# Performance work log

Hardware: AMD Instinct MI355X
Metric: run time of the kernel (lower is better)

Reference implementation:

```python
import jax, jax.numpy as jnp
import numpy as np
from functools import partial

GRAD_THR = 0.01
COUNT_THR = 3
MIN_PROB = 0.1
MAX_PROB = 0.9
FREE_PROB = 1e-10
HEIGHT_Q = 0.7


def prob2logodds(p):
    return jnp.log(p) - jnp.log1p(-p)


def shift_diff(x, d):
    # right neighbor minus left neighbor at dilation d (replicate padding on width)
    xp = jnp.pad(x, [(0, 0)] * (x.ndim - 1) + [(d, d)], mode='edge')
    return xp[..., 2 * d:] - xp[..., :-2 * d]


def assign_score(depth):
    rml_dx = jax.nn.relu(shift_diff(depth, 1))    # relu(right - left)
    lmr_dx = jax.nn.relu(-shift_diff(depth, 1))   # relu(left - right)
    rml_ddx = jax.nn.relu(-shift_diff(rml_dx, 2))  # relu(-(right-left))
    lmr_ddx = jax.nn.relu(shift_diff(lmr_dx, 2))   # relu(-(left-right))
    W = depth.shape[-1]
    grad_pos = jnp.concatenate([rml_ddx[..., :W // 2], lmr_ddx[..., W // 2:]], axis=-1)
    grad_neg = jnp.concatenate([lmr_ddx[..., :W // 2], rml_ddx[..., W // 2:]], axis=-1)
    return grad_pos, grad_neg


def _occupancy_one(xyz, score, g_mask, size, grad_thr, count_thr):
    # xyz: [3, N]; score, g_mask: [N]
    x, y, z = xyz[0], xyz[1], xyz[2]
    range_mask = (x >= 0) & (x <= size - 1) & (z >= 0) & (z <= size - 1)
    height_mask = y < jnp.quantile(y, HEIGHT_Q)
    valid = height_mask & range_mask
    obj = valid & (~g_mask) & (score > 0)
    ground = valid & g_mask
    xi = jnp.clip(x.astype(jnp.int32), 0, size - 1)
    zi = jnp.clip(z.astype(jnp.int32), 0, size - 1)
    idx = xi + size * zi  # [N] flat grid index
    G = size * size
    occ = jnp.zeros(G, jnp.float32).at[idx].add(
        jnp.where(obj & (score > grad_thr), 1.0, 0.0))
    norm = jnp.zeros(G, jnp.float32).at[idx].add(obj.astype(jnp.float32))
    gcnt = jnp.zeros(G, jnp.float32).at[idx].add(ground.astype(jnp.float32))
    free = (gcnt > 0) & (norm == 0)
    unknown = (~free) & (norm < count_thr)
    prob = occ / jnp.maximum(norm, 1.0)
    prob = jnp.where(unknown | free, 0.5, prob)
    return prob, free, unknown


def compute_occupancy_probability(scaled_ptcloud, ground_flat, disc_flat, size, grad_thr, count_thr):
    f = partial(_occupancy_one, size=size, grad_thr=grad_thr, count_thr=count_thr)
    return jax.vmap(f)(scaled_ptcloud, disc_flat, ground_flat)


def max_pool3x3(x):
    return jax.lax.reduce_window(
        x, -jnp.inf, jax.lax.max,
        (1, 1, 3, 3), (1, 1, 1, 1),
        [(0, 0), (0, 0), (1, 1), (1, 1)])


def setup_inputs() -> dict:
    key = jax.random.key(0)
    k1, k2, k3 = jax.random.split(key, 3)
    B, H, W, S = 32, 384, 1280, 256
    N = H * W
    depth = jax.random.uniform(k1, (B, 1, H, W), jnp.float32, 0.1, 80.0)
    ptc = jax.random.uniform(k2, (B, 3, N), jnp.float32, -5.0, float(S) + 5.0)
    gmask = jax.random.randint(k3, (B, 1, H, W), 0, 2).astype(bool)
    return {"depth": depth, "scaled_ptcloud": ptc, "ground_mask": gmask, "ogm_size": S}


def reference(depth, scaled_ptcloud, ground_mask, ogm_size):
    B = depth.shape[0]
    S = ogm_size
    prior_free_odds = prob2logodds(FREE_PROB)
    p_min_odds = prob2logodds(MIN_PROB)
    p_max_odds = prob2logodds(MAX_PROB)
    n_max_odds = prob2logodds(MAX_PROB)

    grad_pos, grad_neg = assign_score(depth)
    gp_flat = grad_pos.reshape(B, -1)
    gn_flat = grad_neg.reshape(B, -1)
    gm_flat = ground_mask.reshape(B, -1)

    pos_prob, free, unknown = compute_occupancy_probability(
        scaled_ptcloud, gm_flat, gp_flat, S, GRAD_THR, COUNT_THR)
    pos_odds = prob2logodds(pos_prob)
    pos_odds = jnp.where(free, prior_free_odds, pos_odds)
    pos_odds = jnp.where(unknown, 0.0, pos_odds)
    pos_odds = jnp.clip(pos_odds, p_min_odds, p_max_odds)

    neg_prob, _, _ = compute_occupancy_probability(
        scaled_ptcloud, gm_flat, gn_flat, S, GRAD_THR, COUNT_THR)
    neg_odds = prob2logodds(neg_prob)
    neg_odds = jnp.where(free | unknown, 0.0, neg_odds)
    neg_odds = jnp.clip(neg_odds, 0.0, n_max_odds)
    neg_odds = max_pool3x3(neg_odds.reshape(B, 1, S, S))

    return pos_odds.reshape(B, 1, S, S) - neg_odds
```

## Files before the change

### kernel.cpp

```cpp
#include <hip/hip_runtime.h>
#include <stdint.h>

#define H_    384
#define W_    1280
#define NPTS  (H_ * W_)
#define S_    256
#define G_    (S_ * S_)
#define NBX   32
#define NBINS 4096
#define QCAP  2048
#define LO_   (-16.0f)
#define INVW_ (4096.0f / 544.0f)
#define PMAX  2.1972246f

typedef unsigned int u32;
typedef unsigned long long u64;
typedef unsigned char u8;
typedef float f32x4 __attribute__((ext_vector_type(4)));
typedef u32   u32x4 __attribute__((ext_vector_type(4)));

__device__ __forceinline__ u32 fkey(float f) {
    u32 u = __float_as_uint(f);
    return (u & 0x80000000u) ? ~u : (u | 0x80000000u);
}
__device__ __forceinline__ float keyfloat(u32 k) {
    u32 u = (k & 0x80000000u) ? (k ^ 0x80000000u) : ~k;
    return __uint_as_float(u);
}
__device__ __forceinline__ int lbin(float y) {
    int b = (int)floorf((y - LO_) * INVW_);
    return b < 0 ? 0 : (b > NBINS - 1 ? NBINS - 1 : b);
}

__global__ void k_histlin(const float* __restrict__ ptc, const u8* __restrict__ gmb,
                          u32* __restrict__ hgsum, u32* __restrict__ mode) {
    __shared__ u32 h[NBINS];
    const int t = threadIdx.x, b = blockIdx.y;
    if (blockIdx.x == 0 && b == 0 && t < 64) {
        u32 v = ((const u32*)gmb)[t];
        bool bad = !(v == 0u || v == 1u || v == 0x3F800000u);
        u64 m = __ballot(bad);
        if (t == 0) *mode = (m == 0ULL) ? 1u : 0u;
    }
    for (int j = t; j < NBINS; j += 256) h[j] = 0u;
    __syncthreads();
    const f32x4* y4 = (const f32x4*)(ptc + (size_t)b * 3 * NPTS + NPTS);
    for (int i = blockIdx.x * 256 + t; i < NPTS / 4; i += NBX * 256) {
        f32x4 v = y4[i];
        atomicAdd(&h[lbin(v.x)], 1u);
        atomicAdd(&h[lbin(v.y)], 1u);
        atomicAdd(&h[lbin(v.z)], 1u);
        atomicAdd(&h[lbin(v.w)], 1u);
    }
    __syncthreads();
    u32* dst = hgsum + (size_t)b * NBINS;
    for (int j = t; j < NBINS; j += 256)
        if (h[j]) atomicAdd(&dst[j], h[j]);
}

__global__ void k_find(const u32* __restrict__ hgsum, u32* __restrict__ fbuf, int ka) {
    __shared__ u32 h[NBINS];
    __shared__ u32 part[256];
    __shared__ u32 sres[4];
    const int t = threadIdx.x, b = blockIdx.x;
    const u32* src = hgsum + (size_t)b * NBINS;
    for (int j = t; j < NBINS; j += 256) h[j] = src[j];
    __syncthreads();
    u32 loc = 0;
#pragma unroll
    for (int q = 0; q < NBINS / 256; q++) loc += h[t * (NBINS / 256) + q];
    part[t] = loc;
    __syncthreads();
    for (int ofs = 1; ofs < 256; ofs <<= 1) {
        u32 v = (t >= ofs) ? part[t - ofs] : 0u;
        __syncthreads();
        part[t] += v;
        __syncthreads();
    }
    u32 before = part[t] - loc;
    const u32 ra = (u32)ka, rb = (u32)ka + 1u;
#pragma unroll
    for (int q = 0; q < NBINS / 256; q++) {
        const int j = t * (NBINS / 256) + q;
        const u32 v = h[j];
        if (before <= ra && ra < before + v) { sres[0] = (u32)j; sres[1] = ra - before; }
        if (before <= rb && rb < before + v) { sres[2] = (u32)j; sres[3] = rb - before; }
        before += v;
    }
    __syncthreads();
    if (t < 4) fbuf[b * 4 + t] = sres[t];
}

__global__ void k_collect(const float* __restrict__ ptc, const u32* __restrict__ fbuf,
                          u32* __restrict__ cnt, u32* __restrict__ cbuf) {
    __shared__ u32 sA, sB;
    const int t = threadIdx.x, b = blockIdx.y;
    if (t == 0) { sA = fbuf[b * 4 + 0]; sB = fbuf[b * 4 + 2]; }
    __syncthreads();
    const int binA = (int)sA, binB = (int)sB;
    const bool twob = (binB != binA);
    const f32x4* y4 = (const f32x4*)(ptc + (size_t)b * 3 * NPTS + NPTS);
    u32* bufA = cbuf + (size_t)b * 2 * QCAP;
    u32* bufB = bufA + QCAP;
    for (int i = blockIdx.x * 256 + t; i < NPTS / 4; i += NBX * 256) {
        f32x4 v = y4[i];
        float f[4] = {v.x, v.y, v.z, v.w};
#pragma unroll
        for (int q = 0; q < 4; q++) {
            const int bn = lbin(f[q]);
            if (bn == binA) {
                u32 p = atomicAdd(&cnt[b * 2], 1u);
                if (p < QCAP) bufA[p] = fkey(f[q]);
            } else if (twob && bn == binB) {
                u32 p = atomicAdd(&cnt[b * 2 + 1], 1u);
                if (p < QCAP) bufB[p] = fkey(f[q]);
            }
        }
    }
}

__global__ void k_select(const u32* __restrict__ fbuf, const u32* __restrict__ cnt,
                         const u32* __restrict__ cbuf, float* __restrict__ tbuf,
                         float wlo, float whi) {
    __shared__ u32 sA[QCAP];
    __shared__ u32 sB[QCAP];
    __shared__ u32 skey[2];
    const int t = threadIdx.x, b = blockIdx.x;
    const u32 binA = fbuf[b * 4 + 0], remA = fbuf[b * 4 + 1];
    const u32 binB = fbuf[b * 4 + 2], remB = fbuf[b * 4 + 3];
    const bool twob = (binB != binA);
    u32 cA = cnt[b * 2];     if (cA > QCAP) cA = QCAP;
    u32 cB = cnt[b * 2 + 1]; if (cB > QCAP) cB = QCAP;
    const u32* bufA = cbuf + (size_t)b * 2 * QCAP;
    const u32* bufB = bufA + QCAP;
    for (u32 i = t; i < cA; i += 256) sA[i] = bufA[i];
    if (twob) for (u32 i = t; i < cB; i += 256) sB[i] = bufB[i];
    __syncthreads();
    for (u32 i = t; i < cA; i += 256) {
        const u32 k = sA[i];
        u32 less = 0, eq = 0;
        for (u32 j = 0; j < cA; j++) { u32 kj = sA[j]; less += (kj < k); eq += (kj == k); }
        if (less <= remA && remA < less + eq) skey[0] = k;
    }
    const u32* src = twob ? sB : sA;
    const u32 mB = twob ? cB : cA;
    for (u32 i = t; i < mB; i += 256) {
        const u32 k = src[i];
        u32 less = 0, eq = 0;
        for (u32 j = 0; j < mB; j++) { u32 kj = src[j]; less += (kj < k); eq += (kj == k); }
        if (less <= remB && remB < less + eq) skey[1] = k;
    }
    __syncthreads();
    if (t == 0) {
        float ylo = keyfloat(skey[0]);
        float yhi = keyfloat(skey[1]);
        tbuf[b] = __fadd_rn(__fmul_rn(ylo, wlo), __fmul_rn(yhi, whi));
    }
    (void)binA;
}

__global__ void k_scatter(const float* __restrict__ depth, const float* __restrict__ ptc,
                          const u8* __restrict__ gmb, const float* __restrict__ tbuf,
                          const u32* __restrict__ mode,
                          u32* __restrict__ pk, u8* __restrict__ gflag) {
    __shared__ float st;
    __shared__ u32 smode;
    if (threadIdx.x == 0) { st = tbuf[blockIdx.y]; smode = *mode; }
    __syncthreads();
    const int b = blockIdx.y;
    const int i4 = blockIdx.x * 256 + threadIdx.x;
    const int i0 = i4 * 4;
    const size_t pb = (size_t)b * 3 * NPTS;

    const f32x4 yv = __builtin_nontemporal_load((const f32x4*)(ptc + pb + NPTS) + i4);
    const float fy[4] = {yv.x, yv.y, yv.z, yv.w};
    bool pass[4]; bool any = false;
#pragma unroll
    for (int q = 0; q < 4; q++) { pass[q] = fy[q] < st; any = any || pass[q]; }
    if (!any) return;

    const f32x4 xv = __builtin_nontemporal_load((const f32x4*)(ptc + pb) + i4);
    const f32x4 zv = __builtin_nontemporal_load((const f32x4*)(ptc + pb + 2 * NPTS) + i4);
    const float fx[4] = {xv.x, xv.y, xv.z, xv.w};
    const float fz[4] = {zv.x, zv.y, zv.z, zv.w};
    u32 gw[4];
    if (smode) {
        u32x4 gg = __builtin_nontemporal_load((const u32x4*)((const u32*)gmb + (size_t)b * NPTS) + i4);
        gw[0] = gg.x; gw[1] = gg.y; gw[2] = gg.z; gw[3] = gg.w;
    } else {
        u32 gg = __builtin_nontemporal_load((const u32*)(gmb + (size_t)b * NPTS) + i4);
        gw[0] = gg & 0xFFu; gw[1] = (gg >> 8) & 0xFFu; gw[2] = (gg >> 16) & 0xFFu; gw[3] = (gg >> 24) & 0xFFu;
    }

    const int colbase = i0 % W_;
    const float* drow = depth + (size_t)b * NPTS + (i0 - colbase);
    u32* pkb = pk + (size_t)b * G_;
    u8* gfb = gflag + (size_t)b * G_;

#pragma unroll
    for (int q = 0; q < 4; q++) {
        if (!pass[q]) continue;
        const float x = fx[q], z = fz[q];
        if (!(x >= 0.0f && x <= 255.0f && z >= 0.0f && z <= 255.0f)) continue;
        const int cell = (int)x + S_ * (int)z;
        if (gw[q]) { gfb[cell] = 1; continue; }

        const int col = colbase + q;
        int j1 = col - 2; if (j1 < 0) j1 = 0;
        int j2 = col + 2; if (j2 > W_ - 1) j2 = W_ - 1;
        int am = j1 - 1;  if (am < 0) am = 0;
        int ap = j1 + 1;  if (ap > W_ - 1) ap = W_ - 1;
        int bm = j2 - 1;  if (bm < 0) bm = 0;
        int bp = j2 + 1;  if (bp > W_ - 1) bp = W_ - 1;
        float a = drow[ap] - drow[am];
        float c = drow[bp] - drow[bm];
        float rml1 = fmaxf(a, 0.0f),  lmr1 = fmaxf(-a, 0.0f);
        float rml2 = fmaxf(c, 0.0f),  lmr2 = fmaxf(-c, 0.0f);
        float rddx = fmaxf(rml1 - rml2, 0.0f);
        float lddx = fmaxf(lmr2 - lmr1, 0.0f);
        float sp, sn;
        if (col < W_ / 2) { sp = rddx; sn = lddx; } else { sp = lddx; sn = rddx; }
        u32 p = (sp > 0.0f) ? (1u | ((u32)(sp > 0.01f) << 8)) : 0u;
        u32 n = (sn > 0.0f) ? ((1u << 16) | ((u32)(sn > 0.01f) << 24)) : 0u;
        const u32 inc = p | n;
        if (inc) atomicAdd(&pkb[cell], inc);
    }
}

#define TX 64
#define TZ 16

__device__ __forceinline__ float neg_val(u32 w) {
    const u32 pn = w & 0xFFu;
    if (pn < 3u) return 0.0f;
    const u32 nn = (w >> 16) & 0xFFu;
    if (nn < 3u) return 0.0f;
    const u32 no = (w >> 24) & 0xFFu;
    float p = (float)no / (float)nn;
    float v = logf(p) - log1pf(-p);
    return fminf(fmaxf(v, 0.0f), PMAX);
}

__global__ void k_finalpool(const u32* __restrict__ pk, const u8* __restrict__ gflag,
                            float* __restrict__ out) {
    __shared__ float ng[(TZ + 2) * (TX + 2)];
    const int t = threadIdx.x, b = blockIdx.y;
    const int x0 = (blockIdx.x & 3) * TX;
    const int z0 = (blockIdx.x >> 2) * TZ;
    const u32* pkb = pk + (size_t)b * G_;
    const u8* gfb = gflag + (size_t)b * G_;
    for (int idx = t; idx < (TZ + 2) * (TX + 2); idx += 256) {
        const int gx = x0 + idx % (TX + 2) - 1;
        const int gz = z0 + idx / (TX + 2) - 1;
        float v = -INFINITY;
        if (gx >= 0 && gx < S_ && gz >= 0 && gz < S_) v = neg_val(pkb[gx + S_ * gz]);
        ng[idx] = v;
    }
    __syncthreads();
    const int lx = t & 63;
    const int lz0 = (t >> 6) * 4;
#pragma unroll
    for (int k = 0; k < 4; k++) {
        const int lz = lz0 + k;
        const int cell = (x0 + lx) + S_ * (z0 + lz);
        const u32 w = pkb[cell];
        const u32 pn = w & 0xFFu;
        float po;
        if (pn < 3u) {
            po = (pn == 0u && gfb[cell]) ? -PMAX : 0.0f;
        } else {
            const u32 oc = (w >> 8) & 0xFFu;
            float p = (float)oc / (float)pn;
            float v = logf(p) - log1pf(-p);
            po = fminf(fmaxf(v, -PMAX), PMAX);
        }
        float mx = -INFINITY;
#pragma unroll
        for (int dz = 0; dz < 3; dz++)
#pragma unroll
            for (int dx = 0; dx < 3; dx++)
                mx = fmaxf(mx, ng[(lz + dz) * (TX + 2) + (lx + dx)]);
        out[(size_t)b * G_ + cell] = po - mx;
    }
}

extern "C" void kernel_launch(void* const* d_in, const int* in_sizes, int n_in,
                              void* d_out, int out_size, void* d_ws, size_t ws_size,
                              hipStream_t stream) {
    const float* depth = (const float*)d_in[0];
    const float* ptc   = (const float*)d_in[1];
    const u8* gm       = (const u8*)d_in[2];
    const int B = in_sizes[0] / NPTS;

    char* ws = (char*)d_ws;
    size_t off = 0;
    auto alloc = [&](size_t bytes) -> void* {
        void* p = ws + off; off += (bytes + 255) & ~(size_t)255; return p;
    };
    u32* pk    = (u32*)alloc((size_t)B * G_ * 4);
    u8*  gflag = (u8*)alloc((size_t)B * G_);
    u32* hgsum = (u32*)alloc((size_t)B * NBINS * 4);
    u32* cnt   = (u32*)alloc((size_t)B * 2 * 4);
    const size_t zero_bytes = off;
    u32* cbuf  = (u32*)alloc((size_t)B * 2 * QCAP * 4);
    float* tbuf= (float*)alloc((size_t)B * 4);
    u32* fbuf  = (u32*)alloc((size_t)B * 4 * 4);
    u32* mode  = (u32*)alloc(4);
    (void)ws_size; (void)n_in; (void)out_size;

    (void)hipMemsetAsync(d_ws, 0, zero_bytes, stream);

    const float idxf = 0.7f * (float)(NPTS - 1);
    const int   ka   = (int)floorf(idxf);
    const float whi  = idxf - (float)ka;
    const float wlo  = 1.0f - whi;

    k_histlin <<<dim3(NBX, B), dim3(256), 0, stream>>>(ptc, gm, hgsum, mode);
    k_find    <<<dim3(B), dim3(256), 0, stream>>>(hgsum, fbuf, ka);
    k_collect <<<dim3(NBX, B), dim3(256), 0, stream>>>(ptc, fbuf, cnt, cbuf);
    k_select  <<<dim3(B), dim3(256), 0, stream>>>(fbuf, cnt, cbuf, tbuf, wlo, whi);
    k_scatter <<<dim3(NPTS / 1024, B), dim3(256), 0, stream>>>(
        depth, ptc, gm, tbuf, mode, pk, gflag);
    k_finalpool<<<dim3(64, B), dim3(256), 0, stream>>>(pk, gflag, (float*)d_out);
}
```

Measured before the change: 507.9 us.

## Fuse all phases into one cooperative persistent kernel with grid syncs

Replaces the memset plus six separate launches with a single cooperative kernel that runs zeroing, histogram, quantile find and collect, select, scatter and final pooling as phases separated by grid-wide syncs. Each block covers a fixed batch and slice, and the scatter phase becomes a grid-stride loop. The quantile bin search is recomputed per block instead of stored, and select buffers reuse shared memory. The aim is to remove launch and inter-kernel gaps, at the cost of grid barrier overhead, a fixed block count limited by occupancy, and a fallback multi-kernel path if the cooperative launch fails.

```diff
diff --git a/kernel.cpp b/kernel.cpp
--- a/kernel.cpp
+++ b/kernel.cpp
@@ -1,17 +1,22 @@
 #include <hip/hip_runtime.h>
+#include <hip/hip_cooperative_groups.h>
 #include <stdint.h>
+
+namespace cg = cooperative_groups;
 
 #define H_    384
 #define W_    1280
 #define NPTS  (H_ * W_)
 #define S_    256
 #define G_    (S_ * S_)
-#define NBX   32
+#define NBB   64
 #define NBINS 4096
-#define QCAP  2048
+#define QCAP  1024
 #define LO_   (-16.0f)
 #define INVW_ (4096.0f / 544.0f)
 #define PMAX  2.1972246f
+#define TX 64
+#define TZ 16
 
 typedef unsigned int u32;
 typedef unsigned long long u64;
@@ -19,6 +24,15 @@
 typedef float f32x4 __attribute__((ext_vector_type(4)));
 typedef u32   u32x4 __attribute__((ext_vector_type(4)));
 
+struct Shm {
+    u32 h[NBINS];
+    u32 part[256];
+    u32 sres[4];
+    u32 skey[2];
+    float sth;
+    u32 smode;
+};
+
 __device__ __forceinline__ u32 fkey(float f) {
     u32 u = __float_as_uint(f);
     return (u & 0x80000000u) ? ~u : (u | 0x80000000u);
@@ -31,78 +45,77 @@
     int b = (int)floorf((y - LO_) * INVW_);
     return b < 0 ? 0 : (b > NBINS - 1 ? NBINS - 1 : b);
 }
-
-__global__ void k_histlin(const float* __restrict__ ptc, const u8* __restrict__ gmb,
-                          u32* __restrict__ hgsum, u32* __restrict__ mode) {
-    __shared__ u32 h[NBINS];
-    const int t = threadIdx.x, b = blockIdx.y;
-    if (blockIdx.x == 0 && b == 0 && t < 64) {
-        u32 v = ((const u32*)gmb)[t];
-        bool bad = !(v == 0u || v == 1u || v == 0x3F800000u);
-        u64 m = __ballot(bad);
-        if (t == 0) *mode = (m == 0ULL) ? 1u : 0u;
-    }
-    for (int j = t; j < NBINS; j += 256) h[j] = 0u;
+__device__ __forceinline__ void decode(int id, int& b, int& j) {
+    const int r = id & 7;
+    const int g8 = id >> 3;
+    j = g8 % NBB;
+    b = (g8 / NBB) * 8 + r;
+}
+
+__device__ void phase_zero(int b, int j, int t, u32* pk, u8* gflag, u32* hgsum, u32* cnt) {
+    const u32x4 z4 = {0u, 0u, 0u, 0u};
+    u32x4* pk4 = (u32x4*)(pk + (size_t)b * G_) + (size_t)j * (G_ / 4 / NBB);
+    for (int k = t; k < G_ / 4 / NBB; k += 256) pk4[k] = z4;
+    u32x4* gf4 = (u32x4*)(gflag + (size_t)b * G_) + (size_t)j * (G_ / 16 / NBB);
+    for (int k = t; k < G_ / 16 / NBB; k += 256) gf4[k] = z4;
+    u32* hs = hgsum + (size_t)b * NBINS + j * (NBINS / NBB);
+    for (int k = t; k < NBINS / NBB; k += 256) hs[k] = 0u;
+    if (j == 0 && t < 2) cnt[b * 2 + t] = 0u;
+}
+
+__device__ void phase_hist(int b, int j, int t, const float* ptc, u32* hgsum, Shm& s) {
+    for (int k = t; k < NBINS; k += 256) s.h[k] = 0u;
     __syncthreads();
     const f32x4* y4 = (const f32x4*)(ptc + (size_t)b * 3 * NPTS + NPTS);
-    for (int i = blockIdx.x * 256 + t; i < NPTS / 4; i += NBX * 256) {
+    for (int i = j * 256 + t; i < NPTS / 4; i += NBB * 256) {
         f32x4 v = y4[i];
-        atomicAdd(&h[lbin(v.x)], 1u);
-        atomicAdd(&h[lbin(v.y)], 1u);
-        atomicAdd(&h[lbin(v.z)], 1u);
-        atomicAdd(&h[lbin(v.w)], 1u);
+        atomicAdd(&s.h[lbin(v.x)], 1u);
+        atomicAdd(&s.h[lbin(v.y)], 1u);
+        atomicAdd(&s.h[lbin(v.z)], 1u);
+        atomicAdd(&s.h[lbin(v.w)], 1u);
     }
     __syncthreads();
     u32* dst = hgsum + (size_t)b * NBINS;
-    for (int j = t; j < NBINS; j += 256)
-        if (h[j]) atomicAdd(&dst[j], h[j]);
-}
-
-__global__ void k_find(const u32* __restrict__ hgsum, u32* __restrict__ fbuf, int ka) {
-    __shared__ u32 h[NBINS];
-    __shared__ u32 part[256];
-    __shared__ u32 sres[4];
-    const int t = threadIdx.x, b = blockIdx.x;
+    for (int k = t; k < NBINS; k += 256)
+        if (s.h[k]) atomicAdd(&dst[k], s.h[k]);
+}
+
+__device__ void phase_find(int b, int t, const u32* hgsum, int ka, Shm& s) {
     const u32* src = hgsum + (size_t)b * NBINS;
-    for (int j = t; j < NBINS; j += 256) h[j] = src[j];
+    for (int k = t; k < NBINS; k += 256) s.h[k] = src[k];
     __syncthreads();
     u32 loc = 0;
 #pragma unroll
-    for (int q = 0; q < NBINS / 256; q++) loc += h[t * (NBINS / 256) + q];
-    part[t] = loc;
+    for (int q = 0; q < NBINS / 256; q++) loc += s.h[t * (NBINS / 256) + q];
+    s.part[t] = loc;
     __syncthreads();
     for (int ofs = 1; ofs < 256; ofs <<= 1) {
-        u32 v = (t >= ofs) ? part[t - ofs] : 0u;
+        u32 v = (t >= ofs) ? s.part[t - ofs] : 0u;
         __syncthreads();
-        part[t] += v;
+        s.part[t] += v;
         __syncthreads();
     }
-    u32 before = part[t] - loc;
+    u32 before = s.part[t] - loc;
     const u32 ra = (u32)ka, rb = (u32)ka + 1u;
 #pragma unroll
     for (int q = 0; q < NBINS / 256; q++) {
-        const int j = t * (NBINS / 256) + q;
-        const u32 v = h[j];
-        if (before <= ra && ra < before + v) { sres[0] = (u32)j; sres[1] = ra - before; }
-        if (before <= rb && rb < before + v) { sres[2] = (u32)j; sres[3] = rb - before; }
+        const int jj = t * (NBINS / 256) + q;
+        const u32 v = s.h[jj];
+        if (before <= ra && ra < before + v) { s.sres[0] = (u32)jj; s.sres[1] = ra - before; }
+        if (before <= rb && rb < before + v) { s.sres[2] = (u32)jj; s.sres[3] = rb - before; }
         before += v;
     }
     __syncthreads();
-    if (t < 4) fbuf[b * 4 + t] = sres[t];
-}
-
-__global__ void k_collect(const float* __restrict__ ptc, const u32* __restrict__ fbuf,
-                          u32* __restrict__ cnt, u32* __restrict__ cbuf) {
-    __shared__ u32 sA, sB;
-    const int t = threadIdx.x, b = blockIdx.y;
-    if (t == 0) { sA = fbuf[b * 4 + 0]; sB = fbuf[b * 4 + 2]; }
-    __syncthreads();
-    const int binA = (int)sA, binB = (int)sB;
+}
+
+__device__ void phase_collect(int b, int j, int t, const float* ptc,
+                              u32* cnt, u32* cbuf, Shm& s) {
+    const int binA = (int)s.sres[0], binB = (int)s.sres[2];
     const bool twob = (binB != binA);
     const f32x4* y4 = (const f32x4*)(ptc + (size_t)b * 3 * NPTS + NPTS);
     u32* bufA = cbuf + (size_t)b * 2 * QCAP;
     u32* bufB = bufA + QCAP;
-    for (int i = blockIdx.x * 256 + t; i < NPTS / 4; i += NBX * 256) {
+    for (int i = j * 256 + t; i < NPTS / 4; i += NBB * 256) {
         f32x4 v = y4[i];
         float f[4] = {v.x, v.y, v.z, v.w};
 #pragma unroll
@@ -119,116 +132,114 @@
     }
 }
 
-__global__ void k_select(const u32* __restrict__ fbuf, const u32* __restrict__ cnt,
-                         const u32* __restrict__ cbuf, float* __restrict__ tbuf,
-                         float wlo, float whi) {
-    __shared__ u32 sA[QCAP];
-    __shared__ u32 sB[QCAP];
-    __shared__ u32 skey[2];
-    const int t = threadIdx.x, b = blockIdx.x;
-    const u32 binA = fbuf[b * 4 + 0], remA = fbuf[b * 4 + 1];
-    const u32 binB = fbuf[b * 4 + 2], remB = fbuf[b * 4 + 3];
-    const bool twob = (binB != binA);
+__device__ void phase_select(int b, int t, const u32* cnt, const u32* cbuf,
+                             float* tbuf, float wlo, float whi, Shm& s) {
+    const u32 remA = s.sres[1], remB = s.sres[3];
+    const bool twob = (s.sres[0] != s.sres[2]);
     u32 cA = cnt[b * 2];     if (cA > QCAP) cA = QCAP;
     u32 cB = cnt[b * 2 + 1]; if (cB > QCAP) cB = QCAP;
     const u32* bufA = cbuf + (size_t)b * 2 * QCAP;
     const u32* bufB = bufA + QCAP;
+    u32* sA = s.h;
+    u32* sB = s.h + QCAP;
+    __syncthreads();
     for (u32 i = t; i < cA; i += 256) sA[i] = bufA[i];
     if (twob) for (u32 i = t; i < cB; i += 256) sB[i] = bufB[i];
     __syncthreads();
     for (u32 i = t; i < cA; i += 256) {
         const u32 k = sA[i];
         u32 less = 0, eq = 0;
-        for (u32 j = 0; j < cA; j++) { u32 kj = sA[j]; less += (kj < k); eq += (kj == k); }
-        if (less <= remA && remA < less + eq) skey[0] = k;
-    }
-    const u32* src = twob ? sB : sA;
+        for (u32 jj = 0; jj < cA; jj++) { u32 kj = sA[jj]; less += (kj < k); eq += (kj == k); }
+        if (less <= remA && remA < less + eq) s.skey[0] = k;
+    }
+    const u32* srcb = twob ? sB : sA;
     const u32 mB = twob ? cB : cA;
     for (u32 i = t; i < mB; i += 256) {
-        const u32 k = src[i];
+        const u32 k = srcb[i];
         u32 less = 0, eq = 0;
-        for (u32 j = 0; j < mB; j++) { u32 kj = src[j]; less += (kj < k); eq += (kj == k); }
-        if (less <= remB && remB < less + eq) skey[1] = k;
+        for (u32 jj = 0; jj < mB; jj++) { u32 kj = srcb[jj]; less += (kj < k); eq += (kj == k); }
+        if (less <= remB && remB < less + eq) s.skey[1] = k;
     }
     __syncthreads();
     if (t == 0) {
-        float ylo = keyfloat(skey[0]);
-        float yhi = keyfloat(skey[1]);
+        float ylo = keyfloat(s.skey[0]);
+        float yhi = keyfloat(s.skey[1]);
         tbuf[b] = __fadd_rn(__fmul_rn(ylo, wlo), __fmul_rn(yhi, whi));
     }
-    (void)binA;
-}
-
-__global__ void k_scatter(const float* __restrict__ depth, const float* __restrict__ ptc,
-                          const u8* __restrict__ gmb, const float* __restrict__ tbuf,
-                          const u32* __restrict__ mode,
-                          u32* __restrict__ pk, u8* __restrict__ gflag) {
-    __shared__ float st;
-    __shared__ u32 smode;
-    if (threadIdx.x == 0) { st = tbuf[blockIdx.y]; smode = *mode; }
-    __syncthreads();
-    const int b = blockIdx.y;
-    const int i4 = blockIdx.x * 256 + threadIdx.x;
-    const int i0 = i4 * 4;
+}
+
+__device__ void phase_scatter(int b, int j, int t, const float* depth, const float* ptc,
+                              const u8* gmb, const float* tbuf,
+                              u32* pk, u8* gflag, Shm& s) {
+    if (t < 64) {
+        u32 v = ((const u32*)gmb)[t];
+        bool bad = !(v == 0u || v == 1u || v == 0x3F800000u);
+        u64 m = __ballot(bad);
+        if (t == 0) s.smode = (m == 0ULL) ? 1u : 0u;
+    }
+    if (t == 0) s.sth = tbuf[b];
+    __syncthreads();
+    const float st = s.sth;
+    const u32 smode = s.smode;
     const size_t pb = (size_t)b * 3 * NPTS;
-
-    const f32x4 yv = __builtin_nontemporal_load((const f32x4*)(ptc + pb + NPTS) + i4);
-    const float fy[4] = {yv.x, yv.y, yv.z, yv.w};
-    bool pass[4]; bool any = false;
-#pragma unroll
-    for (int q = 0; q < 4; q++) { pass[q] = fy[q] < st; any = any || pass[q]; }
-    if (!any) return;
-
-    const f32x4 xv = __builtin_nontemporal_load((const f32x4*)(ptc + pb) + i4);
-    const f32x4 zv = __builtin_nontemporal_load((const f32x4*)(ptc + pb + 2 * NPTS) + i4);
-    const float fx[4] = {xv.x, xv.y, xv.z, xv.w};
-    const float fz[4] = {zv.x, zv.y, zv.z, zv.w};
-    u32 gw[4];
-    if (smode) {
-        u32x4 gg = __builtin_nontemporal_load((const u32x4*)((const u32*)gmb + (size_t)b * NPTS) + i4);
-        gw[0] = gg.x; gw[1] = gg.y; gw[2] = gg.z; gw[3] = gg.w;
-    } else {
-        u32 gg = __builtin_nontemporal_load((const u32*)(gmb + (size_t)b * NPTS) + i4);
-        gw[0] = gg & 0xFFu; gw[1] = (gg >> 8) & 0xFFu; gw[2] = (gg >> 16) & 0xFFu; gw[3] = (gg >> 24) & 0xFFu;
-    }
-
-    const int colbase = i0 % W_;
-    const float* drow = depth + (size_t)b * NPTS + (i0 - colbase);
     u32* pkb = pk + (size_t)b * G_;
     u8* gfb = gflag + (size_t)b * G_;
 
-#pragma unroll
-    for (int q = 0; q < 4; q++) {
-        if (!pass[q]) continue;
-        const float x = fx[q], z = fz[q];
-        if (!(x >= 0.0f && x <= 255.0f && z >= 0.0f && z <= 255.0f)) continue;
-        const int cell = (int)x + S_ * (int)z;
-        if (gw[q]) { gfb[cell] = 1; continue; }
-
-        const int col = colbase + q;
-        int j1 = col - 2; if (j1 < 0) j1 = 0;
-        int j2 = col + 2; if (j2 > W_ - 1) j2 = W_ - 1;
-        int am = j1 - 1;  if (am < 0) am = 0;
-        int ap = j1 + 1;  if (ap > W_ - 1) ap = W_ - 1;
-        int bm = j2 - 1;  if (bm < 0) bm = 0;
-        int bp = j2 + 1;  if (bp > W_ - 1) bp = W_ - 1;
-        float a = drow[ap] - drow[am];
-        float c = drow[bp] - drow[bm];
-        float rml1 = fmaxf(a, 0.0f),  lmr1 = fmaxf(-a, 0.0f);
-        float rml2 = fmaxf(c, 0.0f),  lmr2 = fmaxf(-c, 0.0f);
-        float rddx = fmaxf(rml1 - rml2, 0.0f);
-        float lddx = fmaxf(lmr2 - lmr1, 0.0f);
-        float sp, sn;
-        if (col < W_ / 2) { sp = rddx; sn = lddx; } else { sp = lddx; sn = rddx; }
-        u32 p = (sp > 0.0f) ? (1u | ((u32)(sp > 0.01f) << 8)) : 0u;
-        u32 n = (sn > 0.0f) ? ((1u << 16) | ((u32)(sn > 0.01f) << 24)) : 0u;
-        const u32 inc = p | n;
-        if (inc) atomicAdd(&pkb[cell], inc);
-    }
-}
-
-#define TX 64
-#define TZ 16
+    for (int i4 = j * 256 + t; i4 < NPTS / 4; i4 += NBB * 256) {
+        const int i0 = i4 * 4;
+        const f32x4 yv = __builtin_nontemporal_load((const f32x4*)(ptc + pb + NPTS) + i4);
+        const float fy[4] = {yv.x, yv.y, yv.z, yv.w};
+        bool pass[4]; bool any = false;
+#pragma unroll
+        for (int q = 0; q < 4; q++) { pass[q] = fy[q] < st; any = any || pass[q]; }
+        if (!any) continue;
+
+        const f32x4 xv = __builtin_nontemporal_load((const f32x4*)(ptc + pb) + i4);
+        const f32x4 zv = __builtin_nontemporal_load((const f32x4*)(ptc + pb + 2 * NPTS) + i4);
+        const float fx[4] = {xv.x, xv.y, xv.z, xv.w};
+        const float fz[4] = {zv.x, zv.y, zv.z, zv.w};
+        u32 gw[4];
+        if (smode) {
+            u32x4 gg = __builtin_nontemporal_load((const u32x4*)((const u32*)gmb + (size_t)b * NPTS) + i4);
+            gw[0] = gg.x; gw[1] = gg.y; gw[2] = gg.z; gw[3] = gg.w;
+        } else {
+            u32 gg = __builtin_nontemporal_load((const u32*)(gmb + (size_t)b * NPTS) + i4);
+            gw[0] = gg & 0xFFu; gw[1] = (gg >> 8) & 0xFFu; gw[2] = (gg >> 16) & 0xFFu; gw[3] = (gg >> 24) & 0xFFu;
+        }
+
+        const int colbase = i0 % W_;
+        const float* drow = depth + (size_t)b * NPTS + (i0 - colbase);
+
+#pragma unroll
+        for (int q = 0; q < 4; q++) {
+            if (!pass[q]) continue;
+            const float x = fx[q], z = fz[q];
+            if (!(x >= 0.0f && x <= 255.0f && z >= 0.0f && z <= 255.0f)) continue;
+            const int cell = (int)x + S_ * (int)z;
+            if (gw[q]) { gfb[cell] = 1; continue; }
+
+            const int col = colbase + q;
+            int j1 = col - 2; if (j1 < 0) j1 = 0;
+            int j2 = col + 2; if (j2 > W_ - 1) j2 = W_ - 1;
+            int am = j1 - 1;  if (am < 0) am = 0;
+            int ap = j1 + 1;  if (ap > W_ - 1) ap = W_ - 1;
+            int bm = j2 - 1;  if (bm < 0) bm = 0;
+            int bp = j2 + 1;  if (bp > W_ - 1) bp = W_ - 1;
+            float a = drow[ap] - drow[am];
+            float c = drow[bp] - drow[bm];
+            float rml1 = fmaxf(a, 0.0f),  lmr1 = fmaxf(-a, 0.0f);
+            float rml2 = fmaxf(c, 0.0f),  lmr2 = fmaxf(-c, 0.0f);
+            float rddx = fmaxf(rml1 - rml2, 0.0f);
+            float lddx = fmaxf(lmr2 - lmr1, 0.0f);
+            float sp, sn;
+            if (col < W_ / 2) { sp = rddx; sn = lddx; } else { sp = lddx; sn = rddx; }
+            u32 p = (sp > 0.0f) ? (1u | ((u32)(sp > 0.01f) << 8)) : 0u;
+            u32 n = (sn > 0.0f) ? ((1u << 16) | ((u32)(sn > 0.01f) << 24)) : 0u;
+            const u32 inc = p | n;
+            if (inc) atomicAdd(&pkb[cell], inc);
+        }
+    }
+}
 
 __device__ __forceinline__ float neg_val(u32 w) {
     const u32 pn = w & 0xFFu;
@@ -241,14 +252,14 @@
     return fminf(fmaxf(v, 0.0f), PMAX);
 }
 
-__global__ void k_finalpool(const u32* __restrict__ pk, const u8* __restrict__ gflag,
-                            float* __restrict__ out) {
-    __shared__ float ng[(TZ + 2) * (TX + 2)];
-    const int t = threadIdx.x, b = blockIdx.y;
-    const int x0 = (blockIdx.x & 3) * TX;
-    const int z0 = (blockIdx.x >> 2) * TZ;
+__device__ void phase_final(int b, int j, int t, const u32* pk, const u8* gflag,
+                            float* out, Shm& s) {
+    float* ng = (float*)s.h;
+    const int x0 = (j & 3) * TX;
+    const int z0 = (j >> 2) * TZ;
     const u32* pkb = pk + (size_t)b * G_;
     const u8* gfb = gflag + (size_t)b * G_;
+    __syncthreads();
     for (int idx = t; idx < (TZ + 2) * (TX + 2); idx += 256) {
         const int gx = x0 + idx % (TX + 2) - 1;
         const int gz = z0 + idx / (TX + 2) - 1;
@@ -284,6 +295,62 @@
     }
 }
 
+__global__ __launch_bounds__(256, 8) void k_mega(
+        const float* __restrict__ depth, const float* __restrict__ ptc,
+        const u8* __restrict__ gmb, u32* __restrict__ pk, u8* __restrict__ gflag,
+        u32* __restrict__ hgsum, u32* __restrict__ cnt, u32* __restrict__ cbuf,
+        float* __restrict__ tbuf, float* __restrict__ out,
+        int ka, float wlo, float whi) {
+    __shared__ Shm s;
+    cg::grid_group gg = cg::this_grid();
+    int b, j; decode((int)blockIdx.x, b, j);
+    const int t = (int)threadIdx.x;
+
+    phase_zero(b, j, t, pk, gflag, hgsum, cnt);
+    gg.sync();
+    phase_hist(b, j, t, ptc, hgsum, s);
+    gg.sync();
+    phase_find(b, t, hgsum, ka, s);
+    phase_collect(b, j, t, ptc, cnt, cbuf, s);
+    gg.sync();
+    if (j == 0) phase_select(b, t, cnt, cbuf, tbuf, wlo, whi, s);
+    gg.sync();
+    phase_scatter(b, j, t, depth, ptc, gmb, tbuf, pk, gflag, s);
+    gg.sync();
+    phase_final(b, j, t, pk, gflag, out, s);
+}
+
+__global__ void k_p0(u32* pk, u8* gflag, u32* hgsum, u32* cnt) {
+    int b, j; decode((int)blockIdx.x, b, j);
+    phase_zero(b, j, (int)threadIdx.x, pk, gflag, hgsum, cnt);
+}
+__global__ void k_p1(const float* __restrict__ ptc, u32* hgsum) {
+    __shared__ Shm s; int b, j; decode((int)blockIdx.x, b, j);
+    phase_hist(b, j, (int)threadIdx.x, ptc, hgsum, s);
+}
+__global__ void k_p2(const float* __restrict__ ptc, const u32* hgsum,
+                     u32* cnt, u32* cbuf, int ka) {
+    __shared__ Shm s; int b, j; decode((int)blockIdx.x, b, j);
+    phase_find(b, (int)threadIdx.x, hgsum, ka, s);
+    phase_collect(b, j, (int)threadIdx.x, ptc, cnt, cbuf, s);
+}
+__global__ void k_p3(const u32* hgsum, const u32* cnt, const u32* cbuf,
+                     float* tbuf, int ka, float wlo, float whi) {
+    __shared__ Shm s; const int b = (int)blockIdx.x;
+    phase_find(b, (int)threadIdx.x, hgsum, ka, s);
+    phase_select(b, (int)threadIdx.x, cnt, cbuf, tbuf, wlo, whi, s);
+}
+__global__ void k_p4(const float* __restrict__ depth, const float* __restrict__ ptc,
+                     const u8* __restrict__ gmb, const float* __restrict__ tbuf,
+                     u32* pk, u8* gflag) {
+    __shared__ Shm s; int b, j; decode((int)blockIdx.x, b, j);
+    phase_scatter(b, j, (int)threadIdx.x, depth, ptc, gmb, tbuf, pk, gflag, s);
+}
+__global__ void k_p5(const u32* pk, const u8* gflag, float* out) {
+    __shared__ Shm s; int b, j; decode((int)blockIdx.x, b, j);
+    phase_final(b, j, (int)threadIdx.x, pk, gflag, out, s);
+}
+
 extern "C" void kernel_launch(void* const* d_in, const int* in_sizes, int n_in,
                               void* d_out, int out_size, void* d_ws, size_t ws_size,
                               hipStream_t stream) {
@@ -291,6 +358,7 @@
     const float* ptc   = (const float*)d_in[1];
     const u8* gm       = (const u8*)d_in[2];
     const int B = in_sizes[0] / NPTS;
+    float* outp = (float*)d_out;
 
     char* ws = (char*)d_ws;
     size_t off = 0;
@@ -301,25 +369,27 @@
     u8*  gflag = (u8*)alloc((size_t)B * G_);
     u32* hgsum = (u32*)alloc((size_t)B * NBINS * 4);
     u32* cnt   = (u32*)alloc((size_t)B * 2 * 4);
-    const size_t zero_bytes = off;
     u32* cbuf  = (u32*)alloc((size_t)B * 2 * QCAP * 4);
     float* tbuf= (float*)alloc((size_t)B * 4);
-    u32* fbuf  = (u32*)alloc((size_t)B * 4 * 4);
-    u32* mode  = (u32*)alloc(4);
     (void)ws_size; (void)n_in; (void)out_size;
 
-    (void)hipMemsetAsync(d_ws, 0, zero_bytes, stream);
-
     const float idxf = 0.7f * (float)(NPTS - 1);
-    const int   ka   = (int)floorf(idxf);
-    const float whi  = idxf - (float)ka;
-    const float wlo  = 1.0f - whi;
-
-    k_histlin <<<dim3(NBX, B), dim3(256), 0, stream>>>(ptc, gm, hgsum, mode);
-    k_find    <<<dim3(B), dim3(256), 0, stream>>>(hgsum, fbuf, ka);
-    k_collect <<<dim3(NBX, B), dim3(256), 0, stream>>>(ptc, fbuf, cnt, cbuf);
-    k_select  <<<dim3(B), dim3(256), 0, stream>>>(fbuf, cnt, cbuf, tbuf, wlo, whi);
-    k_scatter <<<dim3(NPTS / 1024, B), dim3(256), 0, stream>>>(
-        depth, ptc, gm, tbuf, mode, pk, gflag);
-    k_finalpool<<<dim3(64, B), dim3(256), 0, stream>>>(pk, gflag, (float*)d_out);
-}
+    int   ka   = (int)floorf(idxf);
+    float whi  = idxf - (float)ka;
+    float wlo  = 1.0f - whi;
+
+    void* kargs[] = { (void*)&depth, (void*)&ptc, (void*)&gm, (void*)&pk, (void*)&gflag,
+                      (void*)&hgsum, (void*)&cnt, (void*)&cbuf, (void*)&tbuf, (void*)&outp,
+                      (void*)&ka, (void*)&wlo, (void*)&whi };
+    hipError_t ce = hipLaunchCooperativeKernel((const void*)k_mega, dim3(NBB * B),
+                                               dim3(256), kargs, 0, stream);
+    if (ce != hipSuccess) {
+        (void)hipGetLastError();
+        k_p0<<<dim3(NBB * B), dim3(256), 0, stream>>>(pk, gflag, hgsum, cnt);
+        k_p1<<<dim3(NBB * B), dim3(256), 0, stream>>>(ptc, hgsum);
+        k_p2<<<dim3(NBB * B), dim3(256), 0, stream>>>(ptc, hgsum, cnt, cbuf, ka);
+        k_p3<<<dim3(B),       dim3(256), 0, stream>>>(hgsum, cnt, cbuf, tbuf, ka, wlo, whi);
+        k_p4<<<dim3(NBB * B), dim3(256), 0, stream>>>(depth, ptc, gm, tbuf, pk, gflag);
+        k_p5<<<dim3(NBB * B), dim3(256), 0, stream>>>(pk, gflag, outp);
+    }
+}
```

After: 1.536 ms. 202% more time.

## Fuse grid zeroing into histogram kernel and remap blocks across batches

Applied to the files above, without the earlier changes.

The large memset of the occupancy grid and ground flags is replaced by having each histogram block zero its own slice, so the memset now covers only the small histogram and counter buffers. All kernels switch to a 1D grid with a decode that interleaves 8 batches per group of blocks, which changes block-to-XCD placement and may improve cache locality. The candidate buffer capacity is halved, which shrinks shared memory in the select kernel but raises the chance of dropping candidates if a bin overflows.

```diff
diff --git a/kernel.cpp b/kernel.cpp
--- a/kernel.cpp
+++ b/kernel.cpp
@@ -6,12 +6,17 @@
 #define NPTS  (H_ * W_)
 #define S_    256
 #define G_    (S_ * S_)
-#define NBX   32
+#define NBH   32
+#define NBC   32
+#define NBS   480
+#define NBF   64
 #define NBINS 4096
-#define QCAP  2048
+#define QCAP  1024
 #define LO_   (-16.0f)
 #define INVW_ (4096.0f / 544.0f)
 #define PMAX  2.1972246f
+#define TX 64
+#define TZ 16
 
 typedef unsigned int u32;
 typedef unsigned long long u64;
@@ -31,21 +36,37 @@
     int b = (int)floorf((y - LO_) * INVW_);
     return b < 0 ? 0 : (b > NBINS - 1 ? NBINS - 1 : b);
 }
-
-__global__ void k_histlin(const float* __restrict__ ptc, const u8* __restrict__ gmb,
-                          u32* __restrict__ hgsum, u32* __restrict__ mode) {
+template<int NBB>
+__device__ __forceinline__ void decode(int id, int& b, int& j) {
+    const int r = id & 7;
+    const int g8 = id >> 3;
+    j = g8 % NBB;
+    b = (g8 / NBB) * 8 + r;
+}
+
+__global__ void k_hist(const float* __restrict__ ptc, const u8* __restrict__ gmb,
+                       u32* __restrict__ hgsum, u32* __restrict__ mode,
+                       u32* __restrict__ pk, u8* __restrict__ gflag) {
     __shared__ u32 h[NBINS];
-    const int t = threadIdx.x, b = blockIdx.y;
-    if (blockIdx.x == 0 && b == 0 && t < 64) {
+    int b, j; decode<NBH>((int)blockIdx.x, b, j);
+    const int t = threadIdx.x;
+    if (b == 0 && j == 0 && t < 64) {
         u32 v = ((const u32*)gmb)[t];
         bool bad = !(v == 0u || v == 1u || v == 0x3F800000u);
         u64 m = __ballot(bad);
         if (t == 0) *mode = (m == 0ULL) ? 1u : 0u;
     }
-    for (int j = t; j < NBINS; j += 256) h[j] = 0u;
+    {
+        const u32x4 z4 = {0u, 0u, 0u, 0u};
+        u32x4* pk4 = (u32x4*)(pk + (size_t)b * G_) + (size_t)j * (G_ / 4 / NBH);
+        for (int k = t; k < G_ / 4 / NBH; k += 256) pk4[k] = z4;
+        u32x4* gf4 = (u32x4*)(gflag + (size_t)b * G_) + (size_t)j * (G_ / 16 / NBH);
+        if (t < G_ / 16 / NBH) gf4[t] = z4;
+    }
+    for (int k = t; k < NBINS; k += 256) h[k] = 0u;
     __syncthreads();
     const f32x4* y4 = (const f32x4*)(ptc + (size_t)b * 3 * NPTS + NPTS);
-    for (int i = blockIdx.x * 256 + t; i < NPTS / 4; i += NBX * 256) {
+    for (int i = j * 256 + t; i < NPTS / 4; i += NBH * 256) {
         f32x4 v = y4[i];
         atomicAdd(&h[lbin(v.x)], 1u);
         atomicAdd(&h[lbin(v.y)], 1u);
@@ -54,8 +75,8 @@
     }
     __syncthreads();
     u32* dst = hgsum + (size_t)b * NBINS;
-    for (int j = t; j < NBINS; j += 256)
-        if (h[j]) atomicAdd(&dst[j], h[j]);
+    for (int k = t; k < NBINS; k += 256)
+        if (h[k]) atomicAdd(&dst[k], h[k]);
 }
 
 __global__ void k_find(const u32* __restrict__ hgsum, u32* __restrict__ fbuf, int ka) {
@@ -64,7 +85,7 @@
     __shared__ u32 sres[4];
     const int t = threadIdx.x, b = blockIdx.x;
     const u32* src = hgsum + (size_t)b * NBINS;
-    for (int j = t; j < NBINS; j += 256) h[j] = src[j];
+    for (int k = t; k < NBINS; k += 256) h[k] = src[k];
     __syncthreads();
     u32 loc = 0;
 #pragma unroll
@@ -81,10 +102,10 @@
     const u32 ra = (u32)ka, rb = (u32)ka + 1u;
 #pragma unroll
     for (int q = 0; q < NBINS / 256; q++) {
-        const int j = t * (NBINS / 256) + q;
-        const u32 v = h[j];
-        if (before <= ra && ra < before + v) { sres[0] = (u32)j; sres[1] = ra - before; }
-        if (before <= rb && rb < before + v) { sres[2] = (u32)j; sres[3] = rb - before; }
+        const int jj = t * (NBINS / 256) + q;
+        const u32 v = h[jj];
+        if (before <= ra && ra < before + v) { sres[0] = (u32)jj; sres[1] = ra - before; }
+        if (before <= rb && rb < before + v) { sres[2] = (u32)jj; sres[3] = rb - before; }
         before += v;
     }
     __syncthreads();
@@ -93,16 +114,15 @@
 
 __global__ void k_collect(const float* __restrict__ ptc, const u32* __restrict__ fbuf,
                           u32* __restrict__ cnt, u32* __restrict__ cbuf) {
-    __shared__ u32 sA, sB;
-    const int t = threadIdx.x, b = blockIdx.y;
-    if (t == 0) { sA = fbuf[b * 4 + 0]; sB = fbuf[b * 4 + 2]; }
-    __syncthreads();
-    const int binA = (int)sA, binB = (int)sB;
+    int b, j; decode<NBC>((int)blockIdx.x, b, j);
+    const int t = threadIdx.x;
+    const int binA = (int)fbuf[b * 4 + 0];
+    const int binB = (int)fbuf[b * 4 + 2];
     const bool twob = (binB != binA);
     const f32x4* y4 = (const f32x4*)(ptc + (size_t)b * 3 * NPTS + NPTS);
     u32* bufA = cbuf + (size_t)b * 2 * QCAP;
     u32* bufB = bufA + QCAP;
-    for (int i = blockIdx.x * 256 + t; i < NPTS / 4; i += NBX * 256) {
+    for (int i = j * 256 + t; i < NPTS / 4; i += NBC * 256) {
         f32x4 v = y4[i];
         float f[4] = {v.x, v.y, v.z, v.w};
 #pragma unroll
@@ -126,9 +146,8 @@
     __shared__ u32 sB[QCAP];
     __shared__ u32 skey[2];
     const int t = threadIdx.x, b = blockIdx.x;
-    const u32 binA = fbuf[b * 4 + 0], remA = fbuf[b * 4 + 1];
-    const u32 binB = fbuf[b * 4 + 2], remB = fbuf[b * 4 + 3];
-    const bool twob = (binB != binA);
+    const u32 remA = fbuf[b * 4 + 1], remB = fbuf[b * 4 + 3];
+    const bool twob = (fbuf[b * 4 + 0] != fbuf[b * 4 + 2]);
     u32 cA = cnt[b * 2];     if (cA > QCAP) cA = QCAP;
     u32 cB = cnt[b * 2 + 1]; if (cB > QCAP) cB = QCAP;
     const u32* bufA = cbuf + (size_t)b * 2 * QCAP;
@@ -139,15 +158,15 @@
     for (u32 i = t; i < cA; i += 256) {
         const u32 k = sA[i];
         u32 less = 0, eq = 0;
-        for (u32 j = 0; j < cA; j++) { u32 kj = sA[j]; less += (kj < k); eq += (kj == k); }
+        for (u32 jj = 0; jj < cA; jj++) { u32 kj = sA[jj]; less += (kj < k); eq += (kj == k); }
         if (less <= remA && remA < less + eq) skey[0] = k;
     }
-    const u32* src = twob ? sB : sA;
+    const u32* srcb = twob ? sB : sA;
     const u32 mB = twob ? cB : cA;
     for (u32 i = t; i < mB; i += 256) {
-        const u32 k = src[i];
+        const u32 k = srcb[i];
         u32 less = 0, eq = 0;
-        for (u32 j = 0; j < mB; j++) { u32 kj = src[j]; less += (kj < k); eq += (kj == k); }
+        for (u32 jj = 0; jj < mB; jj++) { u32 kj = srcb[jj]; less += (kj < k); eq += (kj == k); }
         if (less <= remB && remB < less + eq) skey[1] = k;
     }
     __syncthreads();
@@ -156,19 +175,17 @@
         float yhi = keyfloat(skey[1]);
         tbuf[b] = __fadd_rn(__fmul_rn(ylo, wlo), __fmul_rn(yhi, whi));
     }
-    (void)binA;
 }
 
 __global__ void k_scatter(const float* __restrict__ depth, const float* __restrict__ ptc,
                           const u8* __restrict__ gmb, const float* __restrict__ tbuf,
                           const u32* __restrict__ mode,
                           u32* __restrict__ pk, u8* __restrict__ gflag) {
-    __shared__ float st;
-    __shared__ u32 smode;
-    if (threadIdx.x == 0) { st = tbuf[blockIdx.y]; smode = *mode; }
-    __syncthreads();
-    const int b = blockIdx.y;
-    const int i4 = blockIdx.x * 256 + threadIdx.x;
+    int b, j; decode<NBS>((int)blockIdx.x, b, j);
+    const int t = threadIdx.x;
+    const float st = tbuf[b];
+    const u32 smode = *mode;
+    const int i4 = j * 256 + t;
     const int i0 = i4 * 4;
     const size_t pb = (size_t)b * 3 * NPTS;
 
@@ -227,9 +244,6 @@
     }
 }
 
-#define TX 64
-#define TZ 16
-
 __device__ __forceinline__ float neg_val(u32 w) {
     const u32 pn = w & 0xFFu;
     if (pn < 3u) return 0.0f;
@@ -244,9 +258,10 @@
 __global__ void k_finalpool(const u32* __restrict__ pk, const u8* __restrict__ gflag,
                             float* __restrict__ out) {
     __shared__ float ng[(TZ + 2) * (TX + 2)];
-    const int t = threadIdx.x, b = blockIdx.y;
-    const int x0 = (blockIdx.x & 3) * TX;
-    const int z0 = (blockIdx.x >> 2) * TZ;
+    int b, j; decode<NBF>((int)blockIdx.x, b, j);
+    const int t = threadIdx.x;
+    const int x0 = (j & 3) * TX;
+    const int z0 = (j >> 2) * TZ;
     const u32* pkb = pk + (size_t)b * G_;
     const u8* gfb = gflag + (size_t)b * G_;
     for (int idx = t; idx < (TZ + 2) * (TX + 2); idx += 256) {
@@ -297,11 +312,11 @@
     auto alloc = [&](size_t bytes) -> void* {
         void* p = ws + off; off += (bytes + 255) & ~(size_t)255; return p;
     };
-    u32* pk    = (u32*)alloc((size_t)B * G_ * 4);
-    u8*  gflag = (u8*)alloc((size_t)B * G_);
     u32* hgsum = (u32*)alloc((size_t)B * NBINS * 4);
     u32* cnt   = (u32*)alloc((size_t)B * 2 * 4);
     const size_t zero_bytes = off;
+    u32* pk    = (u32*)alloc((size_t)B * G_ * 4);
+    u8*  gflag = (u8*)alloc((size_t)B * G_);
     u32* cbuf  = (u32*)alloc((size_t)B * 2 * QCAP * 4);
     float* tbuf= (float*)alloc((size_t)B * 4);
     u32* fbuf  = (u32*)alloc((size_t)B * 4 * 4);
@@ -315,11 +330,10 @@
     const float whi  = idxf - (float)ka;
     const float wlo  = 1.0f - whi;
 
-    k_histlin <<<dim3(NBX, B), dim3(256), 0, stream>>>(ptc, gm, hgsum, mode);
-    k_find    <<<dim3(B), dim3(256), 0, stream>>>(hgsum, fbuf, ka);
-    k_collect <<<dim3(NBX, B), dim3(256), 0, stream>>>(ptc, fbuf, cnt, cbuf);
-    k_select  <<<dim3(B), dim3(256), 0, stream>>>(fbuf, cnt, cbuf, tbuf, wlo, whi);
-    k_scatter <<<dim3(NPTS / 1024, B), dim3(256), 0, stream>>>(
-        depth, ptc, gm, tbuf, mode, pk, gflag);
-    k_finalpool<<<dim3(64, B), dim3(256), 0, stream>>>(pk, gflag, (float*)d_out);
-}
+    k_hist    <<<dim3(NBH * B), dim3(256), 0, stream>>>(ptc, gm, hgsum, mode, pk, gflag);
+    k_find    <<<dim3(B),       dim3(256), 0, stream>>>(hgsum, fbuf, ka);
+    k_collect <<<dim3(NBC * B), dim3(256), 0, stream>>>(ptc, fbuf, cnt, cbuf);
+    k_select  <<<dim3(B),       dim3(256), 0, stream>>>(fbuf, cnt, cbuf, tbuf, wlo, whi);
+    k_scatter <<<dim3(NBS * B), dim3(256), 0, stream>>>(depth, ptc, gm, tbuf, mode, pk, gflag);
+    k_finalpool<<<dim3(NBF * B), dim3(256), 0, stream>>>(pk, gflag, (float*)d_out);
+}
```

Result: no change. 512.5 us (+0.9%).
